# Kernel optimization log

Hardware: AMD Instinct MI355X
Metric: run time of the kernel (lower is better)

Reference implementation:

```python
import jax, jax.numpy as jnp
import numpy as np

B, S, D, F, E = 2, 1024, 1024, 4096, 8

def setup_inputs() -> dict:
    key = jax.random.key(0)
    ks = jax.random.split(key, 4)
    s = 0.02
    return {
        "x": jax.random.normal(ks[0], (B, S, D), dtype=jnp.float32),
        "switch_w": jax.random.normal(ks[1], (D, E), dtype=jnp.float32) * s,
        "switch_b": jnp.zeros((E,), dtype=jnp.float32),
        "w1": jax.random.normal(ks[2], (E, D, F), dtype=jnp.float32) * s,
        "b1": jnp.zeros((E, F), dtype=jnp.float32),
        "w2": jax.random.normal(ks[3], (E, F, D), dtype=jnp.float32) * s,
        "b2": jnp.zeros((E, D), dtype=jnp.float32),
    }

def reference(x, switch_w, switch_b, w1, b1, w2, b2):
    b, s, d = x.shape
    xt = x.reshape(-1, d)                               # [T, D]
    logits = xt @ switch_w + switch_b                   # [T, E]
    route_prob = jax.nn.softmax(logits, axis=-1)        # [T, E]
    route_prob_max = jnp.max(route_prob, axis=-1)       # [T]
    routes = jnp.argmax(route_prob, axis=-1)            # [T] int
    onehot = jax.nn.one_hot(routes, E, dtype=xt.dtype)  # [T, E]
    counts = onehot.sum(axis=0)                         # tokens per expert (float, as in torch new_tensor)

    # top-1 dispatch: run each expert FFN, keep only its tokens via mask (drop_tokens=False -> no capacity drop)
    def body(acc, params):
        W1, B1, W2, B2, mask = params                   # mask: [T]
        y = jax.nn.relu(xt @ W1 + B1) @ W2 + B2         # [T, D]
        return acc + mask[:, None] * y, None

    out, _ = jax.lax.scan(body, jnp.zeros_like(xt), (w1, b1, w2, b2, onehot.T))
    out = out * route_prob_max[:, None]                 # is_scale_prob=True
    final_output = out.reshape(b, s, d)
    return final_output, counts, route_prob.sum(axis=0), 0, route_prob_max
```

## Files before the change

kernel.cpp:

```cpp
#include <hip/hip_runtime.h>
#include <stdint.h>

#define T_TOK 2048
#define D_DIM 1024
#define F_DIM 4096
#define E_NUM 8
#define RPMAX 4096
#define BK 64

typedef __attribute__((ext_vector_type(8))) short bfx8;
typedef __attribute__((ext_vector_type(4))) float fx4;

__device__ __forceinline__ unsigned short f2bf(float f) {
  union { float f; uint32_t u; } v; v.f = f;
  uint32_t u = v.u;
  u += 0x7FFFu + ((u >> 16) & 1u);
  return (unsigned short)(u >> 16);
}

__device__ __forceinline__ void load_lds16(const unsigned short* g, unsigned short* l) {
  __builtin_amdgcn_global_load_lds(
      (const __attribute__((address_space(1))) void*)g,
      (__attribute__((address_space(3))) void*)l, 16, 0, 0);
}

__device__ __forceinline__ uint32_t cvtpk_bf16(float lo, float hi) {
  uint32_t d;
  asm("v_cvt_pk_bf16_f32 %0, %1, %2" : "=v"(d) : "v"(lo), "v"(hi));
  return d;
}

__global__ __launch_bounds__(256) void router_kernel(
    const float* __restrict__ x, const float* __restrict__ sw,
    const float* __restrict__ sb, float* __restrict__ pmax_out,
    int* __restrict__ routes, float* __restrict__ probs,
    unsigned short* __restrict__ xbf) {
  const int wave = threadIdx.x >> 6, lane = threadIdx.x & 63;
  const int t = blockIdx.x * 4 + wave;
  const float* xr = x + (size_t)t * D_DIM;
  float acc[8];
#pragma unroll
  for (int e = 0; e < 8; ++e) acc[e] = 0.f;
#pragma unroll
  for (int i = 0; i < 4; ++i) {
    const int d = i * 256 + lane * 4;
    float4 xv = *(const float4*)(xr + d);
    ushort4 h;
    h.x = f2bf(xv.x); h.y = f2bf(xv.y); h.z = f2bf(xv.z); h.w = f2bf(xv.w);
    *(ushort4*)(xbf + (size_t)t * D_DIM + d) = h;
    const float xs[4] = {xv.x, xv.y, xv.z, xv.w};
#pragma unroll
    for (int j = 0; j < 4; ++j) {
      const float4* swp = (const float4*)(sw + (size_t)(d + j) * 8);
      float4 w0 = swp[0], w1 = swp[1];
      acc[0] += xs[j] * w0.x; acc[1] += xs[j] * w0.y;
      acc[2] += xs[j] * w0.z; acc[3] += xs[j] * w0.w;
      acc[4] += xs[j] * w1.x; acc[5] += xs[j] * w1.y;
      acc[6] += xs[j] * w1.z; acc[7] += xs[j] * w1.w;
    }
  }
#pragma unroll
  for (int e = 0; e < 8; ++e) {
    float v = acc[e];
    for (int o = 32; o > 0; o >>= 1) v += __shfl_down(v, o, 64);
    acc[e] = v;
  }
  if (lane == 0) {
#pragma unroll
    for (int e = 0; e < 8; ++e) acc[e] += sb[e];
    int am = 0; float mx = acc[0];
#pragma unroll
    for (int e = 1; e < 8; ++e) if (acc[e] > mx) { mx = acc[e]; am = e; }
    float p[8]; float s = 0.f;
#pragma unroll
    for (int e = 0; e < 8; ++e) { p[e] = expf(acc[e] - mx); s += p[e]; }
    float inv = 1.0f / s;
    pmax_out[t] = inv;
    routes[t] = am;
#pragma unroll
    for (int e = 0; e < 8; ++e) probs[(size_t)t * 8 + e] = p[e] * inv;
  }
}

__global__ __launch_bounds__(256) void plan_kernel(
    const int* __restrict__ routes, const float* __restrict__ probs,
    int* __restrict__ off, int* __restrict__ perm_out, int* __restrict__ perm_src,
    float* __restrict__ out_counts, float* __restrict__ out_psums,
    float* __restrict__ out_zero) {
  __shared__ int cnt[8];
  __shared__ int cur[8];
  __shared__ int offs[9];
  __shared__ float red[256][8];
  const int tid = threadIdx.x;
  if (tid < 8) cnt[tid] = 0;
  for (int i = tid; i < RPMAX; i += 256) { perm_out[i] = -1; perm_src[i] = 0; }
  __syncthreads();
  float loc[8];
#pragma unroll
  for (int e = 0; e < 8; ++e) loc[e] = 0.f;
  for (int t = tid; t < T_TOK; t += 256) {
    atomicAdd(&cnt[routes[t]], 1);
    const float4* p = (const float4*)(probs + (size_t)t * 8);
    float4 a = p[0], b = p[1];
    loc[0] += a.x; loc[1] += a.y; loc[2] += a.z; loc[3] += a.w;
    loc[4] += b.x; loc[5] += b.y; loc[6] += b.z; loc[7] += b.w;
  }
#pragma unroll
  for (int e = 0; e < 8; ++e) red[tid][e] = loc[e];
  __syncthreads();
  for (int s = 128; s >= 1; s >>= 1) {
    if (tid < s) {
#pragma unroll
      for (int e = 0; e < 8; ++e) red[tid][e] += red[tid + s][e];
    }
    __syncthreads();
  }
  if (tid == 0) {
    int o = 0;
    for (int e = 0; e < 8; ++e) { offs[e] = o; o += ((cnt[e] + 255) >> 8) << 8; }
    offs[8] = o;
    *out_zero = 0.0f;
  }
  __syncthreads();
  if (tid < 9) off[tid] = offs[tid];
  if (tid < 8) {
    cur[tid] = offs[tid];
    out_counts[tid] = (float)cnt[tid];
    out_psums[tid] = red[0][tid];
  }
  __syncthreads();
  for (int t = tid; t < T_TOK; t += 256) {
    int e = routes[t];
    int pos = atomicAdd(&cur[e], 1);
    perm_out[pos] = t;
    perm_src[pos] = t;
  }
}

__global__ __launch_bounds__(256) void gather_kernel(
    const unsigned short* __restrict__ xbf, const int* __restrict__ off,
    const int* __restrict__ perm_src, unsigned short* __restrict__ xg) {
  const int wave = threadIdx.x >> 6, lane = threadIdx.x & 63;
  const int row = blockIdx.x * 4 + wave;
  if (row >= off[8]) return;
  const int tok = perm_src[row];
  const bfx8* s = (const bfx8*)(xbf + (size_t)tok * D_DIM);
  bfx8* d = (bfx8*)(xg + (size_t)row * D_DIM);
  d[lane] = s[lane];
  d[lane + 64] = s[lane + 64];
}

__global__ __launch_bounds__(256) void reduce_kernel(
    const float* __restrict__ P, const int* __restrict__ off,
    const int* __restrict__ perm_out, const float* __restrict__ b2,
    const float* __restrict__ pmax, float* __restrict__ out) {
  const int row = blockIdx.x;
  if (row >= off[8]) return;
  const int tok = perm_out[row];
  if (tok < 0) return;
  int e = 0;
#pragma unroll
  for (int i = 1; i <= 7; ++i) if (row >= off[i]) e = i;
  const int col = threadIdx.x * 4;
  const size_t base = (size_t)row * D_DIM + col;
  float4 p0 = *(const float4*)(P + base);
  float4 p1 = *(const float4*)(P + (size_t)1 * RPMAX * D_DIM + base);
  float4 p2 = *(const float4*)(P + (size_t)2 * RPMAX * D_DIM + base);
  float4 p3 = *(const float4*)(P + (size_t)3 * RPMAX * D_DIM + base);
  float4 bv = *(const float4*)(b2 + (size_t)e * D_DIM + col);
  const float pm = pmax[tok];
  float4 r;
  r.x = (p0.x + p1.x + p2.x + p3.x + bv.x) * pm;
  r.y = (p0.y + p1.y + p2.y + p3.y + bv.y) * pm;
  r.z = (p0.z + p1.z + p2.z + p3.z + bv.z) * pm;
  r.w = (p0.w + p1.w + p2.w + p3.w + bv.w) * pm;
  *(float4*)(out + (size_t)tok * D_DIM + col) = r;
}

template <int BN, int K_, int N_, int KSPLIT, bool FIRST>
__global__ __launch_bounds__(512, 2) void gemm256(
    const unsigned short* __restrict__ A,
    const float* __restrict__ W,
    const float* __restrict__ Bias,
    const int* __restrict__ off,
    unsigned short* __restrict__ Hout, float* __restrict__ Pout) {
  constexpr int BM = 256;
  constexpr int KS = K_ / KSPLIT;
  constexpr int NT = KS / BK;
  constexpr int FM = 8;
  constexpr int FN = BN / 64;
  constexpr int GRP = BN / 128;
  constexpr int NBX = N_ / BN;
  __shared__ __align__(16) unsigned short As[2][BM * 64];
  __shared__ __align__(16) unsigned short Bs[2][BN * 64];
  const int tid = threadIdx.x;
  const int nby = gridDim.y;
  const int lin = (blockIdx.z * nby + blockIdx.y) * NBX + blockIdx.x;
  const int total = NBX * nby * KSPLIT;
  const int newlin = (lin & 7) * (total >> 3) + (lin >> 3);
  const int bx = newlin / (nby * KSPLIT);
  const int rem = newlin % (nby * KSPLIT);
  const int by = rem % nby;
  const int kz = rem / nby;
  const int rowbase = by * BM;
  if (rowbase >= off[8]) return;
  int e = 0;
#pragma unroll
  for (int i = 1; i <= 7; ++i) if (rowbase >= off[i]) e = i;
  const int n0 = bx * BN;
  const int k0base = kz * KS;
  const int wave = tid >> 6, lane = tid & 63;
  const int wm = wave >> 2, wn = wave & 3;
  const float* Wn0 = W + (size_t)e * K_ * N_ + n0;

  const unsigned short* aSrc[4];
#pragma unroll
  for (int c = 0; c < 4; ++c) {
    int ca = (wave * 4 + c) * 64 + lane;
    int row = ca >> 3, slot = ca & 7;
    int sc = slot ^ (row & 7);
    aSrc[c] = A + (size_t)(rowbase + row) * K_ + k0base + sc * 8;
  }

  const int nq = lane & 15;
  const int qg = lane >> 4;
  const int kq = (qg & 1) * 4;
  fx4 br[GRP][4];

  auto A_STAGE = [&](int kt, unsigned short* Asb) {
#pragma unroll
    for (int c = 0; c < 4; ++c)
      load_lds16(aSrc[c] + kt, Asb + (wave * 4 + c) * 512);
  };
  auto B_LOAD = [&](int kt) {
#pragma unroll
    for (int g = 0; g < GRP; ++g) {
      const int cb = g * 2 + (qg >> 1);
#pragma unroll
      for (int j = 0; j < 4; ++j)
        br[g][j] = *(const fx4*)(Wn0 + (size_t)(kt + wave * 8 + kq + j) * N_ +
                                 cb * 64 + nq * 4);
    }
  };
  auto B_STORE = [&](unsigned short* Bsb) {
#pragma unroll
    for (int g = 0; g < GRP; ++g) {
      const int cb = g * 2 + (qg >> 1);
#pragma unroll
      for (int i = 0; i < 4; ++i) {
        const int nl = cb * 64 + nq * 4 + i;
        const int key = ((nl >> 2) + 2 * (nl & 3)) & 7;
        uint32_t d0 = cvtpk_bf16(br[g][0][i], br[g][1][i]);
        uint32_t d1 = cvtpk_bf16(br[g][2][i], br[g][3][i]);
        *(uint2*)(Bsb + nl * 64 + (wave ^ key) * 8 + kq) = make_uint2(d0, d1);
      }
    }
  };

  fx4 acc[FM][FN];
#pragma unroll
  for (int a = 0; a < FM; ++a)
#pragma unroll
    for (int b = 0; b < FN; ++b) acc[a][b] = (fx4){0.f, 0.f, 0.f, 0.f};

  auto COMPUTE = [&](const unsigned short* Asb, const unsigned short* Bsb) {
#pragma unroll
    for (int kk = 0; kk < 2; ++kk) {
      bfx8 af[FM], bf[FN];
#pragma unroll
      for (int fm = 0; fm < FM; ++fm) {
        int r = wm * 128 + fm * 16 + (lane & 15);
        int c = (kk * 4 + (lane >> 4)) ^ (r & 7);
        af[fm] = *(const bfx8*)(Asb + r * 64 + c * 8);
      }
#pragma unroll
      for (int fn = 0; fn < FN; ++fn) {
        int nn = wn * (BN / 4) + fn * 16 + (lane & 15);
        int key = ((nn >> 2) + 2 * (nn & 3)) & 7;
        int c = (kk * 4 + (lane >> 4)) ^ key;
        bf[fn] = *(const bfx8*)(Bsb + nn * 64 + c * 8);
      }
#pragma unroll
      for (int fm = 0; fm < FM; ++fm)
#pragma unroll
        for (int fn = 0; fn < FN; ++fn)
          acc[fm][fn] = __builtin_amdgcn_mfma_f32_16x16x32_bf16(
              af[fm], bf[fn], acc[fm][fn], 0, 0, 0);
    }
  };

  A_STAGE(0, As[0]);
  B_LOAD(0);
  B_STORE(Bs[0]);
  __syncthreads();

  for (int t = 0; t < NT; ++t) {
    const int c = t & 1;
    if (t + 1 < NT) {
      A_STAGE((t + 1) * BK, As[c ^ 1]);
      B_LOAD((t + 1) * BK);
    }
    COMPUTE(As[c], Bs[c]);
    if (t + 1 < NT) B_STORE(Bs[c ^ 1]);
    __syncthreads();
  }

  const int colbase = n0 + wn * (BN / 4);
  if (FIRST) {
#pragma unroll
    for (int fn = 0; fn < FN; ++fn) {
      int colg = colbase + fn * 16 + (lane & 15);
      float bv = Bias[(size_t)e * N_ + colg];
#pragma unroll
      for (int fm = 0; fm < FM; ++fm) {
        int rg = rowbase + wm * 128 + fm * 16 + ((lane >> 4) << 2);
#pragma unroll
        for (int j = 0; j < 4; ++j) {
          float v = fmaxf(acc[fm][fn][j] + bv, 0.f);
          Hout[(size_t)(rg + j) * N_ + colg] = f2bf(v);
        }
      }
    }
  } else {
    float* Pk = Pout + (size_t)kz * RPMAX * N_;
#pragma unroll
    for (int fm = 0; fm < FM; ++fm) {
      int rg = rowbase + wm * 128 + fm * 16 + ((lane >> 4) << 2);
#pragma unroll
      for (int j = 0; j < 4; ++j) {
#pragma unroll
        for (int fn = 0; fn < FN; ++fn) {
          int colg = colbase + fn * 16 + (lane & 15);
          Pk[(size_t)(rg + j) * N_ + colg] = acc[fm][fn][j];
        }
      }
    }
  }
}

extern "C" void kernel_launch(void* const* d_in, const int* in_sizes, int n_in,
                              void* d_out, int out_size, void* d_ws, size_t ws_size,
                              hipStream_t stream) {
  const float* x  = (const float*)d_in[0];
  const float* sw = (const float*)d_in[1];
  const float* sb = (const float*)d_in[2];
  const float* w1 = (const float*)d_in[3];
  const float* b1 = (const float*)d_in[4];
  const float* w2 = (const float*)d_in[5];
  const float* b2 = (const float*)d_in[6];
  float* out = (float*)d_out;

  char* ws = (char*)d_ws;
  int*   off      = (int*)(ws + 0);
  int*   routes   = (int*)(ws + 1024);
  int*   perm_out = (int*)(ws + 16384);
  int*   perm_src = (int*)(ws + 32768);
  float* probs    = (float*)(ws + 65536);
  unsigned short* xbf = (unsigned short*)(ws + (1u << 20));
  unsigned short* H   = (unsigned short*)(ws + (8u << 20));
  unsigned short* xg  = (unsigned short*)(ws + (40u << 20));
  float* P            = (float*)(ws + (48u << 20));

  float* out_final  = out;
  float* out_counts = out + 2097152;
  float* out_psums  = out + 2097160;
  float* out_zero   = out + 2097168;
  float* out_pmax   = out + 2097169;

  router_kernel<<<T_TOK / 4, 256, 0, stream>>>(x, sw, sb, out_pmax, routes, probs, xbf);
  plan_kernel<<<1, 256, 0, stream>>>(routes, probs, off, perm_out, perm_src,
                                     out_counts, out_psums, out_zero);
  gather_kernel<<<RPMAX / 4, 256, 0, stream>>>(xbf, off, perm_src, xg);

  gemm256<256, D_DIM, F_DIM, 1, true>
      <<<dim3(F_DIM / 256, RPMAX / 256, 1), 512, 0, stream>>>(
          xg, w1, b1, off, H, nullptr);
  gemm256<256, F_DIM, D_DIM, 4, false>
      <<<dim3(D_DIM / 256, RPMAX / 256, 4), 512, 0, stream>>>(
          H, w2, b2, off, nullptr, P);
  reduce_kernel<<<RPMAX, 256, 0, stream>>>(P, off, perm_out, b2, out_pmax, out_final);
}
```

Baseline: 135.8 us.

## Use smaller-tile single-buffered split-K kernel for second expert GEMM

Replaces the second GEMM (H @ W2, split-K by 4) with a dedicated kernel using 128-row tiles, single-buffered LDS, and launch bounds targeting 4 blocks per CU instead of 2. The smaller M tile doubles the block count and cuts LDS and registers per block, aiming to raise occupancy so other resident blocks hide memory latency instead of explicit double buffering. In exchange each W2 tile is loaded and converted from fp32 more often per output, and software pipelining within a block is lost.

```diff
diff --git a/kernel.cpp b/kernel.cpp
--- a/kernel.cpp
+++ b/kernel.cpp
@@ -180,8 +180,7 @@
 template <int BN, int K_, int N_, int KSPLIT, bool FIRST>
 __global__ __launch_bounds__(512, 2) void gemm256(
     const unsigned short* __restrict__ A,
-    const float* __restrict__ W,
-    const float* __restrict__ Bias,
+    const float* __restrict__ W, const float* __restrict__ Bias,
     const int* __restrict__ off,
     unsigned short* __restrict__ Hout, float* __restrict__ Pout) {
   constexpr int BM = 256;
@@ -338,6 +337,127 @@
   }
 }
 
+template <int K_, int N_, int KSPLIT>
+__global__ __launch_bounds__(512, 4) void gemm2s(
+    const unsigned short* __restrict__ A,
+    const float* __restrict__ W,
+    const int* __restrict__ off,
+    float* __restrict__ Pout) {
+  constexpr int BM = 128, BN = 256;
+  constexpr int KS = K_ / KSPLIT;
+  constexpr int NT = KS / BK;
+  constexpr int FM = 4, FN = 4, GRP = 2;
+  constexpr int NBX = N_ / BN;
+  __shared__ __align__(16) unsigned short As[BM * 64];
+  __shared__ __align__(16) unsigned short Bs[BN * 64];
+  const int tid = threadIdx.x;
+  const int nby = gridDim.y;
+  const int lin = (blockIdx.z * nby + blockIdx.y) * NBX + blockIdx.x;
+  const int total = NBX * nby * KSPLIT;
+  const int newlin = (lin & 7) * (total >> 3) + (lin >> 3);
+  const int bx = newlin / (nby * KSPLIT);
+  const int rem = newlin % (nby * KSPLIT);
+  const int by = rem % nby;
+  const int kz = rem / nby;
+  const int rowbase = by * BM;
+  if (rowbase >= off[8]) return;
+  int e = 0;
+#pragma unroll
+  for (int i = 1; i <= 7; ++i) if (rowbase >= off[i]) e = i;
+  const int n0 = bx * BN;
+  const int k0base = kz * KS;
+  const int wave = tid >> 6, lane = tid & 63;
+  const int wm = wave >> 2, wn = wave & 3;
+  const float* Wn0 = W + (size_t)e * K_ * N_ + n0;
+
+  const unsigned short* aSrc[2];
+#pragma unroll
+  for (int c = 0; c < 2; ++c) {
+    int ca = (wave * 2 + c) * 64 + lane;
+    int row = ca >> 3, slot = ca & 7;
+    int sc = slot ^ (row & 7);
+    aSrc[c] = A + (size_t)(rowbase + row) * K_ + k0base + sc * 8;
+  }
+
+  const int nq = lane & 15;
+  const int qg = lane >> 4;
+  const int kq = (qg & 1) * 4;
+  fx4 br[GRP][4];
+
+  fx4 acc[FM][FN];
+#pragma unroll
+  for (int a = 0; a < FM; ++a)
+#pragma unroll
+    for (int b = 0; b < FN; ++b) acc[a][b] = (fx4){0.f, 0.f, 0.f, 0.f};
+
+  for (int t = 0; t < NT; ++t) {
+    const int kt = t * BK;
+#pragma unroll
+    for (int c = 0; c < 2; ++c)
+      load_lds16(aSrc[c] + kt, As + (wave * 2 + c) * 512);
+#pragma unroll
+    for (int g = 0; g < GRP; ++g) {
+      const int cb = g * 2 + (qg >> 1);
+#pragma unroll
+      for (int j = 0; j < 4; ++j)
+        br[g][j] = *(const fx4*)(Wn0 + (size_t)(kt + wave * 8 + kq + j) * N_ +
+                                 cb * 64 + nq * 4);
+    }
+#pragma unroll
+    for (int g = 0; g < GRP; ++g) {
+      const int cb = g * 2 + (qg >> 1);
+#pragma unroll
+      for (int i = 0; i < 4; ++i) {
+        const int nl = cb * 64 + nq * 4 + i;
+        const int key = ((nl >> 2) + 2 * (nl & 3)) & 7;
+        uint32_t d0 = cvtpk_bf16(br[g][0][i], br[g][1][i]);
+        uint32_t d1 = cvtpk_bf16(br[g][2][i], br[g][3][i]);
+        *(uint2*)(Bs + nl * 64 + (wave ^ key) * 8 + kq) = make_uint2(d0, d1);
+      }
+    }
+    __syncthreads();
+#pragma unroll
+    for (int kk = 0; kk < 2; ++kk) {
+      bfx8 af[FM], bf[FN];
+#pragma unroll
+      for (int fm = 0; fm < FM; ++fm) {
+        int r = wm * 64 + fm * 16 + (lane & 15);
+        int c = (kk * 4 + (lane >> 4)) ^ (r & 7);
+        af[fm] = *(const bfx8*)(As + r * 64 + c * 8);
+      }
+#pragma unroll
+      for (int fn = 0; fn < FN; ++fn) {
+        int nn = wn * 64 + fn * 16 + (lane & 15);
+        int key = ((nn >> 2) + 2 * (nn & 3)) & 7;
+        int c = (kk * 4 + (lane >> 4)) ^ key;
+        bf[fn] = *(const bfx8*)(Bs + nn * 64 + c * 8);
+      }
+#pragma unroll
+      for (int fm = 0; fm < FM; ++fm)
+#pragma unroll
+        for (int fn = 0; fn < FN; ++fn)
+          acc[fm][fn] = __builtin_amdgcn_mfma_f32_16x16x32_bf16(
+              af[fm], bf[fn], acc[fm][fn], 0, 0, 0);
+    }
+    __syncthreads();
+  }
+
+  const int colbase = n0 + wn * 64;
+  float* Pk = Pout + (size_t)kz * RPMAX * N_;
+#pragma unroll
+  for (int fm = 0; fm < FM; ++fm) {
+    int rg = rowbase + wm * 64 + fm * 16 + ((lane >> 4) << 2);
+#pragma unroll
+    for (int j = 0; j < 4; ++j) {
+#pragma unroll
+      for (int fn = 0; fn < FN; ++fn) {
+        int colg = colbase + fn * 16 + (lane & 15);
+        Pk[(size_t)(rg + j) * N_ + colg] = acc[fm][fn][j];
+      }
+    }
+  }
+}
+
 extern "C" void kernel_launch(void* const* d_in, const int* in_sizes, int n_in,
                               void* d_out, int out_size, void* d_ws, size_t ws_size,
                               hipStream_t stream) {
@@ -375,8 +495,7 @@
   gemm256<256, D_DIM, F_DIM, 1, true>
       <<<dim3(F_DIM / 256, RPMAX / 256, 1), 512, 0, stream>>>(
           xg, w1, b1, off, H, nullptr);
-  gemm256<256, F_DIM, D_DIM, 4, false>
-      <<<dim3(D_DIM / 256, RPMAX / 256, 4), 512, 0, stream>>>(
-          H, w2, b2, off, nullptr, P);
+  gemm2s<F_DIM, D_DIM, 4>
+      <<<dim3(D_DIM / 256, RPMAX / 128, 4), 512, 0, stream>>>(H, w2, off, P);
   reduce_kernel<<<RPMAX, 256, 0, stream>>>(P, off, perm_out, b2, out_pmax, out_final);
 }
```

Result: faster. 132.7 us (-2.3%).
